# Kernel tuning notes

Hardware: AMD Instinct MI355X
Metric: run time of the kernel (lower is better)

The kernel has to match this reference:

```python
import jax, jax.numpy as jnp
import numpy as np

N_CODES = 1024
CODE_DIM = 256
DECAY = 0.99
EPS = 1e-05


def setup_inputs() -> dict:
    key = jax.random.key(0)
    k1, k2, k3, k4 = jax.random.split(key, 4)
    z = jax.random.normal(k1, (32, CODE_DIM, 32, 32), dtype=jnp.float32)
    embed = jax.random.normal(k2, (N_CODES, CODE_DIM), dtype=jnp.float32)
    cluster_size = jax.random.uniform(k3, (N_CODES,), dtype=jnp.float32)
    embed_avg = jax.random.normal(k4, (N_CODES, CODE_DIM), dtype=jnp.float32)
    return {"z": z, "embed": embed, "cluster_size": cluster_size, "embed_avg": embed_avg}


def reference(z, embed, cluster_size, embed_avg):
    B, D, H, W = z.shape
    K = embed.shape[0]
    # (B*H*W, D) tokens
    flat = jnp.transpose(z, (0, 2, 3, 1)).reshape(-1, D)
    distances = (
        jnp.sum(flat * flat, axis=1, keepdims=True)
        - 2.0 * flat @ embed.T
        + jnp.sum(embed * embed, axis=1)[None, :]
    )
    indices = jnp.argmin(distances, axis=1)  # (N,)
    z_q = embed[indices].reshape(B, H, W, D).transpose(0, 3, 1, 2)  # (B, D, H, W)

    # EMA codebook update (training mode), no onehot materialization
    cs = jax.ops.segment_sum(jnp.ones(flat.shape[0], dtype=flat.dtype), indices, num_segments=K)
    es = jax.ops.segment_sum(flat, indices, num_segments=K)
    new_cluster_size = cluster_size * DECAY + (1.0 - DECAY) * cs
    new_embed_avg = embed_avg * DECAY + (1.0 - DECAY) * es
    n = jnp.sum(new_cluster_size)
    cs_norm = (new_cluster_size + EPS) / (n + K * EPS) * n
    new_embed = new_embed_avg / cs_norm[:, None]

    # straight-through estimator
    z_q_st = z + jax.lax.stop_gradient(z_q - z)
    # torch: F.mse_loss(z.detach(), z_q) -> grads flow to z_q (codebook) only
    vq_loss = jnp.mean((jax.lax.stop_gradient(z) - z_q) ** 2)
    return (z_q_st, indices.reshape(B, H, W), vq_loss, new_embed, new_cluster_size, new_embed_avg)
```

## Files before the change

### kernel.cpp

```cpp
#include <hip/hip_runtime.h>
#include <stdint.h>

#define DECAY 0.99f
#define OMDECAY 0.01f
#define EPSV 1e-5f


typedef _Float16 half8 __attribute__((ext_vector_type(8)));
typedef float floatx4 __attribute__((ext_vector_type(4)));

typedef __attribute__((address_space(1))) const uint32_t gu32;
typedef __attribute__((address_space(3))) uint32_t lu32;

__device__ __forceinline__ void gld16(uint32_t* l, const uint32_t* g) {
    __builtin_amdgcn_global_load_lds((gu32*)g, (lu32*)l, 16, 0, 0);
}

__device__ __forceinline__ uint32_t pack_hl(float v) {
    _Float16 h = (_Float16)v;
    _Float16 lo = (_Float16)(v - (float)h);
    return (uint32_t)__builtin_bit_cast(unsigned short, h) |
           ((uint32_t)__builtin_bit_cast(unsigned short, lo) << 16);
}

__device__ __forceinline__ unsigned int encf(float s) {
    unsigned int b = __builtin_bit_cast(unsigned int, s);
    return (b & 0x80000000u) ? ~b : (b | 0x80000000u);
}

__global__ void prep_embed(const float* __restrict__ embed,
                           unsigned short* __restrict__ B_hi16,
                           unsigned short* __restrict__ B_lo16,
                           float* __restrict__ enorm,
                           float* __restrict__ cs ,
                           uint32_t* __restrict__ b64i) {
    __shared__ float ws4[4];
    const int k = blockIdx.x;
    const int tid = threadIdx.x;
    const int lane = tid & 63;
    const int wv = tid >> 6;
    int idx = k * 256 + tid;
    float v = embed[idx];
    _Float16 h = (_Float16)v;
    _Float16 lo = (_Float16)(v - (float)h);
    B_hi16[idx] = __builtin_bit_cast(unsigned short, h);
    B_lo16[idx] = __builtin_bit_cast(unsigned short, lo);
    float s = v * v;
    for (int off = 32; off > 0; off >>= 1) s += __shfl_down(s, off);
    if (lane == 0) ws4[wv] = s;
    __syncthreads();
    if (tid == 0) enorm[k] = ws4[0] + ws4[1] + ws4[2] + ws4[3];
    if (k < 256) b64i[k * 256 + tid] = 0xFFFFFFFFu;
    if (k == 0) {
        for (int i = tid; i < 2048; i += 256) cs[i] = 0.f;
    }
}

__global__ void split_z(const float* __restrict__ z,
                        uint32_t* __restrict__ A_hi32,
                        uint32_t* __restrict__ A_lo32) {
    __shared__ uint32_t sp[32 * 258];
    const int lane = threadIdx.x & 63;
    const int wv   = threadIdx.x >> 6;
    const int t0   = blockIdx.x * 32;
    const int b    = t0 >> 10;
    const int hw0  = t0 & 1023;
    const int l32  = lane & 31;
    const int dh   = lane >> 5;

    for (int dp = wv; dp < 128; dp += 4) {
        int dd = dp * 2 + dh;
        float v = z[b * 262144 + dd * 1024 + hw0 + l32];
        sp[l32 * 258 + dd] = pack_hl(v);
    }
    __syncthreads();
    for (int r = wv; r < 32; r += 4) {
#pragma unroll
        for (int h2 = 0; h2 < 2; ++h2) {
            int dpair = h2 * 64 + lane;
            uint32_t u0 = sp[r * 258 + 2 * dpair];
            uint32_t u1 = sp[r * 258 + 2 * dpair + 1];
            A_hi32[(t0 + r) * 128 + dpair] = (u0 & 0xffffu) | (u1 << 16);
            A_lo32[(t0 + r) * 128 + dpair] = (u0 >> 16) | (u1 & 0xffff0000u);
        }
    }
}

__global__ __launch_bounds__(256, 2) void vq_mfma(
    const uint32_t* __restrict__ A_hi32,
    const uint32_t* __restrict__ A_lo32,
    const uint32_t* __restrict__ B_hi32,
    const uint32_t* __restrict__ B_lo32,
    const float* __restrict__ enorm,
    unsigned long long* __restrict__ best64)
{
    __shared__ __align__(16) _Float16 AsH[128 * 32];
    __shared__ __align__(16) _Float16 AsL[128 * 32];
    __shared__ __align__(16) _Float16 BsH[256 * 32];
    __shared__ __align__(16) _Float16 BsL[256 * 32];

    const int lane = threadIdx.x & 63;
    const int w    = threadIdx.x >> 6;
    const int q    = lane >> 4;
    const int c16  = lane & 15;
    const int t0   = (blockIdx.x >> 1) * 128;
    const int cb   = (blockIdx.x & 1) * 512;
    const int lane4 = lane >> 2;
    const int dd8   = (lane & 3) * 8;

    for (int nc = 0; nc < 2; ++nc) {
        floatx4 acc[8][4];
#pragma unroll
        for (int i = 0; i < 8; ++i)
#pragma unroll
            for (int j = 0; j < 4; ++j)
                acc[i][j] = (floatx4){0.f, 0.f, 0.f, 0.f};

        for (int dc = 0; dc < 8; ++dc) {
            const int d0 = dc * 32;
            __syncthreads();
            for (int s = w; s < 48; s += 4) {
                if (s < 16) {
                    int ss = s & 7;
                    const uint32_t* base = (s < 8) ? A_hi32 : A_lo32;
                    uint32_t* dst = (uint32_t*)((s < 8) ? AsH : AsL) + ss * 256;
                    int tok = ss * 16 + lane4;
                    gld16(dst, base + (t0 + tok) * 128 + ((d0 + dd8) >> 1));
                } else {
                    int sb = s - 16;
                    int ss = sb & 15;
                    const uint32_t* base = (sb < 16) ? B_hi32 : B_lo32;
                    uint32_t* dst = (uint32_t*)((sb < 16) ? BsH : BsL) + ss * 256;
                    int code = cb + nc * 256 + ss * 16 + lane4;
                    gld16(dst, base + code * 128 + ((d0 + dd8) >> 1));
                }
            }
            __syncthreads();

            half8 bH[4], bL[4];
#pragma unroll
            for (int j = 0; j < 4; ++j) {
                int off = (w * 64 + j * 16 + c16) * 32 + q * 8;
                bH[j] = *(const half8*)(BsH + off);
                bL[j] = *(const half8*)(BsL + off);
            }
#pragma unroll
            for (int i = 0; i < 8; ++i) {
                int off = (i * 16 + c16) * 32 + q * 8;
                half8 aH = *(const half8*)(AsH + off);
                half8 aL = *(const half8*)(AsL + off);
#pragma unroll
                for (int j = 0; j < 4; ++j) {
                    acc[i][j] = __builtin_amdgcn_mfma_f32_16x16x32_f16(aH, bH[j], acc[i][j], 0, 0, 0);
                    acc[i][j] = __builtin_amdgcn_mfma_f32_16x16x32_f16(aH, bL[j], acc[i][j], 0, 0, 0);
                    acc[i][j] = __builtin_amdgcn_mfma_f32_16x16x32_f16(aL, bH[j], acc[i][j], 0, 0, 0);
                }
            }
        }

        float bestv[32];
        int   besti[32];
#pragma unroll
        for (int s = 0; s < 32; ++s) { bestv[s] = 3.4e38f; besti[s] = 0; }
#pragma unroll
        for (int j = 0; j < 4; ++j) {
            int code = cb + nc * 256 + w * 64 + j * 16 + c16;
            float en = enorm[code];
#pragma unroll
            for (int i = 0; i < 8; ++i)
#pragma unroll
                for (int r = 0; r < 4; ++r) {
                    float sc = en - 2.0f * acc[i][j][r];
                    int slot = i * 4 + r;
                    if (sc < bestv[slot] || (sc == bestv[slot] && code < besti[slot])) {
                        bestv[slot] = sc; besti[slot] = code;
                    }
                }
        }
#pragma unroll
        for (int slot = 0; slot < 32; ++slot) {
            float v = bestv[slot]; int bi = besti[slot];
#pragma unroll
            for (int m = 1; m < 16; m <<= 1) {
                float ov = __shfl_xor(v, m);
                int   oi = __shfl_xor(bi, m);
                if (ov < v || (ov == v && oi < bi)) { v = ov; bi = oi; }
            }
            bestv[slot] = v; besti[slot] = bi;
        }
#pragma unroll
        for (int slot = 0; slot < 32; ++slot) {
            if (c16 == (slot & 15)) {
                int tok = (slot >> 2) * 16 + q * 4 + (slot & 3);
                unsigned long long key =
                    ((unsigned long long)encf(bestv[slot]) << 32) |
                    (unsigned int)besti[slot];
                atomicMin(&best64[t0 + tok], key);
            }
        }
    }
}

__global__ __launch_bounds__(256) void merge_zq(
    const unsigned long long* __restrict__ best64,
    const float* __restrict__ z,
    const float* __restrict__ embed,
    float* __restrict__ out_zq,
    float* __restrict__ out_idx,
    float* __restrict__ cs,
    float* __restrict__ loss_sum)
{
    __shared__ int sidx[128];
    const int tid = threadIdx.x;
    const int lane = tid & 63;
    const int w = tid >> 6;
    const int t0 = blockIdx.x * 128;

    if (tid < 128) {
        int bi = (int)(unsigned int)(best64[t0 + tid] & 0xffffffffULL);
        sidx[tid] = bi;
        out_idx[t0 + tid] = (float)bi;
        atomicAdd(&cs[bi], 1.0f);
    }
    __syncthreads();

    const int b_idx = t0 >> 10;
    const int hw0   = t0 & 1023;
    const int zbase = b_idx * 262144 + hw0;
    const int ka = sidx[lane];
    const int kb = sidx[lane + 64];
    float lsum = 0.f;
    for (int d = w; d < 256; d += 4) {
        float zv0 = z[zbase + d * 1024 + lane];
        float zv1 = z[zbase + d * 1024 + lane + 64];
        float e0 = embed[ka * 256 + d];
        float e1 = embed[kb * 256 + d];
        out_zq[zbase + d * 1024 + lane]      = zv0 + (e0 - zv0);
        out_zq[zbase + d * 1024 + lane + 64] = zv1 + (e1 - zv1);
        float d0f = zv0 - e0, d1f = zv1 - e1;
        lsum += d0f * d0f + d1f * d1f;
    }
    for (int off = 32; off > 0; off >>= 1) lsum += __shfl_down(lsum, off);
    if (lane == 0) atomicAdd(loss_sum, lsum);
}

__global__ void vq_finalize_small(const float* __restrict__ cluster_size,
                                  const float* __restrict__ cs,
                                  const float* __restrict__ loss_sum,
                                  float* __restrict__ out_loss,
                                  float* __restrict__ out_ncs,
                                  float* __restrict__ csnorm,
                                  int* __restrict__ offsets,
                                  int* __restrict__ cursor)
{
    __shared__ float wsum[16];
    __shared__ float wncs[16];
    __shared__ float stot[1];
    const int k = threadIdx.x;
    const int lane = k & 63;
    const int wv = k >> 6;
    float cnt = cs[k];
    float ncs = cluster_size[k] * DECAY + OMDECAY * cnt;
    out_ncs[k] = ncs;
    float sc = cnt;
#pragma unroll
    for (int d = 1; d < 64; d <<= 1) {
        float up = __shfl_up(sc, d);
        if (lane >= d) sc += up;
    }
    if (lane == 63) wsum[wv] = sc;
    float ns = ncs;
    for (int off = 32; off > 0; off >>= 1) ns += __shfl_down(ns, off);
    if (lane == 0) wncs[wv] = ns;
    __syncthreads();
    if (wv == 0) {
        float v = (lane < 16) ? wsum[lane] : 0.f;
#pragma unroll
        for (int d = 1; d < 16; d <<= 1) {
            float up = __shfl_up(v, d);
            if (lane >= d) v += up;
        }
        if (lane < 16) wsum[lane] = v;
    } else if (wv == 1) {
        float t = (lane < 16) ? wncs[lane] : 0.f;
        for (int off = 32; off > 0; off >>= 1) t += __shfl_down(t, off);
        if (lane == 0) stot[0] = t;
    }
    __syncthreads();
    float incl = sc + (wv ? wsum[wv - 1] : 0.f);
    int excl = __float2int_rn(incl - cnt);
    offsets[k] = excl;
    cursor[k]  = excl;
    float n = stot[0];
    csnorm[k] = (ncs + EPSV) / (n + 1024.0f * EPSV) * n;
    if (k == 0) out_loss[0] = loss_sum[0] / 8388608.0f;
}

__global__ void scatter_perm(const float* __restrict__ out_idx,
                             int* __restrict__ cursor,
                             int* __restrict__ perm,
                             float* __restrict__ es)
{
    int t = blockIdx.x * 256 + threadIdx.x;
#pragma unroll
    for (int i = 0; i < 8; ++i) es[t + i * 32768] = 0.f;
    int code = (int)out_idx[t];
    int pos = atomicAdd(&cursor[code], 1);
    perm[pos] = t;
}

__global__ void es_sum(const uint32_t* __restrict__ A_hi32,
                       const uint32_t* __restrict__ A_lo32,
                       const int* __restrict__ perm,
                       const float* __restrict__ out_idx,
                       float* __restrict__ es)
{
    __shared__ int sperm[32];
    __shared__ int scode[32];
    const int base = blockIdx.x * 32;
    const int tid = threadIdx.x;
    const int j = tid & 127;
    const uint32_t* __restrict__ A = (tid >> 7) ? A_lo32 : A_hi32;
    if (tid < 32) {
        int t = perm[base + tid];
        sperm[tid] = t;
        scode[tid] = (int)out_idx[t];
    }
    __syncthreads();

    float s0 = 0.f, s1 = 0.f;
    int cur = scode[0];
    uint32_t pu[2];
    pu[0] = A[sperm[0] * 128 + j];
    pu[1] = A[sperm[1] * 128 + j];
#pragma unroll
    for (int i = 0; i < 32; ++i) {
        uint32_t u = pu[i & 1];
        if (i + 2 < 32) pu[i & 1] = A[sperm[i + 2] * 128 + j];
        int code = scode[i];
        if (code != cur) {
            atomicAdd(&es[cur * 256 + 2 * j],     s0);
            atomicAdd(&es[cur * 256 + 2 * j + 1], s1);
            s0 = 0.f; s1 = 0.f; cur = code;
        }
        s0 += (float)__builtin_bit_cast(_Float16, (unsigned short)(u & 0xffffu));
        s1 += (float)__builtin_bit_cast(_Float16, (unsigned short)(u >> 16));
    }
    atomicAdd(&es[cur * 256 + 2 * j],     s0);
    atomicAdd(&es[cur * 256 + 2 * j + 1], s1);
}

__global__ void finalize_embed(const float* __restrict__ embed_avg,
                               const float* __restrict__ es,
                               const float* __restrict__ csnorm,
                               float* __restrict__ out_embed,
                               float* __restrict__ out_nea)
{
    int idx = blockIdx.x * 256 + threadIdx.x;
    int k = idx >> 8;
    float nea = embed_avg[idx] * DECAY + OMDECAY * es[idx];
    out_nea[idx] = nea;
    out_embed[idx] = nea / csnorm[k];
}

extern "C" void kernel_launch(void* const* d_in, const int* in_sizes, int n_in,
                              void* d_out, int out_size, void* d_ws, size_t ws_size,
                              hipStream_t stream) {
    const float* z            = (const float*)d_in[0];
    const float* embed        = (const float*)d_in[1];
    const float* cluster_size = (const float*)d_in[2];
    const float* embed_avg    = (const float*)d_in[3];
    float* out = (float*)d_out;
    uint32_t* ws32 = (uint32_t*)d_ws;

    uint32_t* B_hi32 = ws32 + 0;
    uint32_t* B_lo32 = ws32 + 131072;
    uint32_t* A_hi32 = ws32 + 262144;
    uint32_t* A_lo32 = ws32 + 4456448;
    int* perm        = (int*)(ws32 + 8650752);
    int* offsets     = (int*)(ws32 + 8683520);
    int* cursor      = (int*)(ws32 + 8684544);
    float* cs        = (float*)(ws32 + 8912896);
    float* loss_sum  = (float*)(ws32 + 8913920);
    float* enorm     = (float*)(ws32 + 8914944);
    float* csnorm    = (float*)(ws32 + 8915968);
    float* es        = (float*)(ws32 + 0);
    unsigned long long* best64 = (unsigned long long*)(out + 8421378);

    prep_embed<<<1024, 256, 0, stream>>>(embed, (unsigned short*)B_hi32,
                                         (unsigned short*)B_lo32, enorm, cs,
                                         (uint32_t*)best64);
    split_z<<<1024, 256, 0, stream>>>(z, A_hi32, A_lo32);
    vq_mfma<<<512, 256, 0, stream>>>(A_hi32, A_lo32, B_hi32, B_lo32, enorm, best64);
    merge_zq<<<256, 256, 0, stream>>>(best64, z, embed,
                                      out, out + 8388608, cs, loss_sum);
    vq_finalize_small<<<1, 1024, 0, stream>>>(cluster_size, cs, loss_sum,
                                              out + 8421376, out + 8683521, csnorm,
                                              offsets, cursor);
    scatter_perm<<<128, 256, 0, stream>>>(out + 8388608, cursor, perm, es);
    es_sum<<<1024, 256, 0, stream>>>(A_hi32, A_lo32, perm, out + 8388608, es);
    finalize_embed<<<1024, 256, 0, stream>>>(embed_avg, es, csnorm,
                                             out + 8421377, out + 8684545);
}
```

Before: 270.4 us.

## Double-buffer LDS tiles in VQ MFMA kernel with 512-thread blocks and swizzle

```diff
diff --git a/kernel.cpp b/kernel.cpp
--- a/kernel.cpp
+++ b/kernel.cpp
@@ -86,7 +86,7 @@
     }
 }
 
-__global__ __launch_bounds__(256, 2) void vq_mfma(
+__global__ __launch_bounds__(512, 2) void vq_mfma(
     const uint32_t* __restrict__ A_hi32,
     const uint32_t* __restrict__ A_lo32,
     const uint32_t* __restrict__ B_hi32,
@@ -94,83 +94,108 @@
     const float* __restrict__ enorm,
     unsigned long long* __restrict__ best64)
 {
-    __shared__ __align__(16) _Float16 AsH[128 * 32];
-    __shared__ __align__(16) _Float16 AsL[128 * 32];
-    __shared__ __align__(16) _Float16 BsH[256 * 32];
-    __shared__ __align__(16) _Float16 BsL[256 * 32];
-
-    const int lane = threadIdx.x & 63;
-    const int w    = threadIdx.x >> 6;
-    const int q    = lane >> 4;
-    const int c16  = lane & 15;
-    const int t0   = (blockIdx.x >> 1) * 128;
-    const int cb   = (blockIdx.x & 1) * 512;
+    __shared__ __align__(16) _Float16 lds[2][4][8192];
+
+    const int lane  = threadIdx.x & 63;
+    const int w     = threadIdx.x >> 6;
+    const int wh    = w >> 2;
+    const int wj    = w & 3;
+    const int q     = lane >> 4;
+    const int c16   = lane & 15;
+    const int t0    = (blockIdx.x >> 1) * 256;
+    const int cb    = (blockIdx.x & 1) * 512;
     const int lane4 = lane >> 2;
-    const int dd8   = (lane & 3) * 8;
-
+    const int dd8s  = ((lane & 3) ^ ((lane >> 3) & 3)) * 8;
+    const int qs    = q ^ ((c16 >> 1) & 3);
+
+    const int m = w >> 1;
+    const uint32_t* const sbase =
+        (m == 0) ? A_hi32 : (m == 1) ? A_lo32 : (m == 2) ? B_hi32 : B_lo32;
+    const bool isA = (m < 2);
+
+    float en[2][4];
+#pragma unroll
+    for (int nc = 0; nc < 2; ++nc)
+#pragma unroll
+        for (int j = 0; j < 4; ++j)
+            en[nc][j] = enorm[cb + nc * 256 + wj * 64 + j * 16 + c16];
+
+    floatx4 acc[8][4];
+#pragma unroll
+    for (int i = 0; i < 8; ++i)
+#pragma unroll
+        for (int j = 0; j < 4; ++j)
+            acc[i][j] = (floatx4){0.f, 0.f, 0.f, 0.f};
+
+    auto STAGE = [&](int step) {
+        const int buf = step & 1;
+        const int ncs = (step >> 3) & 1;
+        const int d0  = (step & 7) * 32;
+        const int srcoff = (d0 + dd8s) >> 1;
+        const int rowb = isA ? t0 : (cb + ncs * 256);
+        uint32_t* dst0 = (uint32_t*)(&lds[buf][m][0]);
+#pragma unroll
+        for (int s8 = 0; s8 < 8; ++s8) {
+            const int r16 = (w & 1) * 8 + s8;
+            const int row = rowb + r16 * 16 + lane4;
+            gld16(dst0 + r16 * 256, sbase + row * 128 + srcoff);
+        }
+    };
+
+    STAGE(0);
+
+#pragma unroll
     for (int nc = 0; nc < 2; ++nc) {
-        floatx4 acc[8][4];
-#pragma unroll
-        for (int i = 0; i < 8; ++i)
-#pragma unroll
-            for (int j = 0; j < 4; ++j)
-                acc[i][j] = (floatx4){0.f, 0.f, 0.f, 0.f};
-
         for (int dc = 0; dc < 8; ++dc) {
-            const int d0 = dc * 32;
-            __syncthreads();
-            for (int s = w; s < 48; s += 4) {
-                if (s < 16) {
-                    int ss = s & 7;
-                    const uint32_t* base = (s < 8) ? A_hi32 : A_lo32;
-                    uint32_t* dst = (uint32_t*)((s < 8) ? AsH : AsL) + ss * 256;
-                    int tok = ss * 16 + lane4;
-                    gld16(dst, base + (t0 + tok) * 128 + ((d0 + dd8) >> 1));
-                } else {
-                    int sb = s - 16;
-                    int ss = sb & 15;
-                    const uint32_t* base = (sb < 16) ? B_hi32 : B_lo32;
-                    uint32_t* dst = (uint32_t*)((sb < 16) ? BsH : BsL) + ss * 256;
-                    int code = cb + nc * 256 + ss * 16 + lane4;
-                    gld16(dst, base + code * 128 + ((d0 + dd8) >> 1));
+            const int s = nc * 8 + dc;
+            STAGE((s + 1) & 15);
+            asm volatile("s_waitcnt vmcnt(8)" ::: "memory");
+            __builtin_amdgcn_s_barrier();
+            asm volatile("" ::: "memory");
+
+            const _Float16* pAH = &lds[s & 1][0][0];
+            const _Float16* pAL = &lds[s & 1][1][0];
+            const _Float16* pBH = &lds[s & 1][2][0];
+            const _Float16* pBL = &lds[s & 1][3][0];
+
+            half8 bH[4], bL[4];
+#pragma unroll
+            for (int j = 0; j < 4; ++j) {
+                const int off = (wj * 64 + j * 16 + c16) * 32 + qs * 8;
+                bH[j] = *(const half8*)(pBH + off);
+                bL[j] = *(const half8*)(pBL + off);
+            }
+            __builtin_amdgcn_s_setprio(1);
+#pragma unroll
+            for (int i = 0; i < 8; ++i) {
+                const int off = (wh * 128 + i * 16 + c16) * 32 + qs * 8;
+                half8 vaH = *(const half8*)(pAH + off);
+                half8 vaL = *(const half8*)(pAL + off);
+#pragma unroll
+                for (int j = 0; j < 4; ++j) {
+                    acc[i][j] = __builtin_amdgcn_mfma_f32_16x16x32_f16(vaH, bH[j], acc[i][j], 0, 0, 0);
+                    acc[i][j] = __builtin_amdgcn_mfma_f32_16x16x32_f16(vaH, bL[j], acc[i][j], 0, 0, 0);
+                    acc[i][j] = __builtin_amdgcn_mfma_f32_16x16x32_f16(vaL, bH[j], acc[i][j], 0, 0, 0);
                 }
             }
-            __syncthreads();
-
-            half8 bH[4], bL[4];
-#pragma unroll
-            for (int j = 0; j < 4; ++j) {
-                int off = (w * 64 + j * 16 + c16) * 32 + q * 8;
-                bH[j] = *(const half8*)(BsH + off);
-                bL[j] = *(const half8*)(BsL + off);
-            }
-#pragma unroll
-            for (int i = 0; i < 8; ++i) {
-                int off = (i * 16 + c16) * 32 + q * 8;
-                half8 aH = *(const half8*)(AsH + off);
-                half8 aL = *(const half8*)(AsL + off);
-#pragma unroll
-                for (int j = 0; j < 4; ++j) {
-                    acc[i][j] = __builtin_amdgcn_mfma_f32_16x16x32_f16(aH, bH[j], acc[i][j], 0, 0, 0);
-                    acc[i][j] = __builtin_amdgcn_mfma_f32_16x16x32_f16(aH, bL[j], acc[i][j], 0, 0, 0);
-                    acc[i][j] = __builtin_amdgcn_mfma_f32_16x16x32_f16(aL, bH[j], acc[i][j], 0, 0, 0);
-                }
-            }
+            __builtin_amdgcn_s_setprio(0);
+            asm volatile("" ::: "memory");
+            __builtin_amdgcn_s_barrier();
         }
 
         float bestv[32];
         int   besti[32];
 #pragma unroll
-        for (int s = 0; s < 32; ++s) { bestv[s] = 3.4e38f; besti[s] = 0; }
+        for (int sl = 0; sl < 32; ++sl) { bestv[sl] = 3.4e38f; besti[sl] = 0; }
 #pragma unroll
         for (int j = 0; j < 4; ++j) {
-            int code = cb + nc * 256 + w * 64 + j * 16 + c16;
-            float en = enorm[code];
+            const int code = cb + nc * 256 + wj * 64 + j * 16 + c16;
+            const float enj = en[nc][j];
 #pragma unroll
             for (int i = 0; i < 8; ++i)
 #pragma unroll
                 for (int r = 0; r < 4; ++r) {
-                    float sc = en - 2.0f * acc[i][j][r];
+                    float sc = enj - 2.0f * acc[i][j][r];
                     int slot = i * 4 + r;
                     if (sc < bestv[slot] || (sc == bestv[slot] && code < besti[slot])) {
                         bestv[slot] = sc; besti[slot] = code;
@@ -181,9 +206,9 @@
         for (int slot = 0; slot < 32; ++slot) {
             float v = bestv[slot]; int bi = besti[slot];
 #pragma unroll
-            for (int m = 1; m < 16; m <<= 1) {
-                float ov = __shfl_xor(v, m);
-                int   oi = __shfl_xor(bi, m);
+            for (int mm = 1; mm < 16; mm <<= 1) {
+                float ov = __shfl_xor(v, mm);
+                int   oi = __shfl_xor(bi, mm);
                 if (ov < v || (ov == v && oi < bi)) { v = ov; bi = oi; }
             }
             bestv[slot] = v; besti[slot] = bi;
@@ -191,12 +216,19 @@
 #pragma unroll
         for (int slot = 0; slot < 32; ++slot) {
             if (c16 == (slot & 15)) {
-                int tok = (slot >> 2) * 16 + q * 4 + (slot & 3);
+                int tok = t0 + wh * 128 + (slot >> 2) * 16 + q * 4 + (slot & 3);
                 unsigned long long key =
                     ((unsigned long long)encf(bestv[slot]) << 32) |
                     (unsigned int)besti[slot];
-                atomicMin(&best64[t0 + tok], key);
+                atomicMin(&best64[tok], key);
             }
+        }
+        if (nc == 0) {
+#pragma unroll
+            for (int i = 0; i < 8; ++i)
+#pragma unroll
+                for (int j = 0; j < 4; ++j)
+                    acc[i][j] = (floatx4){0.f, 0.f, 0.f, 0.f};
         }
     }
 }
@@ -391,7 +423,7 @@
                                          (unsigned short*)B_lo32, enorm, cs,
                                          (uint32_t*)best64);
     split_z<<<1024, 256, 0, stream>>>(z, A_hi32, A_lo32);
-    vq_mfma<<<512, 256, 0, stream>>>(A_hi32, A_lo32, B_hi32, B_lo32, enorm, best64);
+    vq_mfma<<<256, 512, 0, stream>>>(A_hi32, A_lo32, B_hi32, B_lo32, enorm, best64);
     merge_zq<<<256, 256, 0, stream>>>(best64, z, embed,
                                       out, out + 8388608, cs, loss_sum);
     vq_finalize_small<<<1, 1024, 0, stream>>>(cluster_size, cs, loss_sum,
```

Measured after the change: 266.2 us. No clear change (-1.5%).

## Restructure VQ distance GEMM with double-buffered A, register B, and XCD-aware mapping

Applied to the files above, without the earlier changes.

```diff
diff --git a/kernel.cpp b/kernel.cpp
--- a/kernel.cpp
+++ b/kernel.cpp
@@ -28,60 +28,60 @@
     return (b & 0x80000000u) ? ~b : (b | 0x80000000u);
 }
 
-__global__ void prep_embed(const float* __restrict__ embed,
+__global__ void prep_fused(const float* __restrict__ z,
+                           uint32_t* __restrict__ A_hi32,
+                           uint32_t* __restrict__ A_lo32,
+                           const float* __restrict__ embed,
                            unsigned short* __restrict__ B_hi16,
                            unsigned short* __restrict__ B_lo16,
                            float* __restrict__ enorm,
                            float* __restrict__ cs ,
                            uint32_t* __restrict__ b64i) {
-    __shared__ float ws4[4];
-    const int k = blockIdx.x;
+    __shared__ uint32_t sp[32 * 258];
+    const int bx = blockIdx.x;
     const int tid = threadIdx.x;
     const int lane = tid & 63;
     const int wv = tid >> 6;
-    int idx = k * 256 + tid;
-    float v = embed[idx];
-    _Float16 h = (_Float16)v;
-    _Float16 lo = (_Float16)(v - (float)h);
-    B_hi16[idx] = __builtin_bit_cast(unsigned short, h);
-    B_lo16[idx] = __builtin_bit_cast(unsigned short, lo);
-    float s = v * v;
-    for (int off = 32; off > 0; off >>= 1) s += __shfl_down(s, off);
-    if (lane == 0) ws4[wv] = s;
-    __syncthreads();
-    if (tid == 0) enorm[k] = ws4[0] + ws4[1] + ws4[2] + ws4[3];
-    if (k < 256) b64i[k * 256 + tid] = 0xFFFFFFFFu;
-    if (k == 0) {
-        for (int i = tid; i < 2048; i += 256) cs[i] = 0.f;
-    }
-}
-
-__global__ void split_z(const float* __restrict__ z,
-                        uint32_t* __restrict__ A_hi32,
-                        uint32_t* __restrict__ A_lo32) {
-    __shared__ uint32_t sp[32 * 258];
-    const int lane = threadIdx.x & 63;
-    const int wv   = threadIdx.x >> 6;
-    const int t0   = blockIdx.x * 32;
-    const int b    = t0 >> 10;
-    const int hw0  = t0 & 1023;
-    const int l32  = lane & 31;
-    const int dh   = lane >> 5;
-
-    for (int dp = wv; dp < 128; dp += 4) {
-        int dd = dp * 2 + dh;
-        float v = z[b * 262144 + dd * 1024 + hw0 + l32];
-        sp[l32 * 258 + dd] = pack_hl(v);
-    }
-    __syncthreads();
-    for (int r = wv; r < 32; r += 4) {
-#pragma unroll
-        for (int h2 = 0; h2 < 2; ++h2) {
-            int dpair = h2 * 64 + lane;
-            uint32_t u0 = sp[r * 258 + 2 * dpair];
-            uint32_t u1 = sp[r * 258 + 2 * dpair + 1];
-            A_hi32[(t0 + r) * 128 + dpair] = (u0 & 0xffffu) | (u1 << 16);
-            A_lo32[(t0 + r) * 128 + dpair] = (u0 >> 16) | (u1 & 0xffff0000u);
+
+    if (bx < 1024) {
+        const int t0  = bx * 32;
+        const int b   = t0 >> 10;
+        const int hw0 = t0 & 1023;
+        const int l32 = lane & 31;
+        const int dh  = lane >> 5;
+        for (int dp = wv; dp < 128; dp += 4) {
+            int dd = dp * 2 + dh;
+            float v = z[b * 262144 + dd * 1024 + hw0 + l32];
+            sp[l32 * 258 + dd] = pack_hl(v);
+        }
+        __syncthreads();
+        for (int r = wv; r < 32; r += 4) {
+#pragma unroll
+            for (int h2 = 0; h2 < 2; ++h2) {
+                int dpair = h2 * 64 + lane;
+                uint32_t u0 = sp[r * 258 + 2 * dpair];
+                uint32_t u1 = sp[r * 258 + 2 * dpair + 1];
+                A_hi32[(t0 + r) * 128 + dpair] = (u0 & 0xffffu) | (u1 << 16);
+                A_lo32[(t0 + r) * 128 + dpair] = (u0 >> 16) | (u1 & 0xffff0000u);
+            }
+        }
+    } else {
+        float* ws4 = (float*)sp;
+        const int k = bx - 1024;
+        int idx = k * 256 + tid;
+        float v = embed[idx];
+        _Float16 h = (_Float16)v;
+        _Float16 lo = (_Float16)(v - (float)h);
+        B_hi16[idx] = __builtin_bit_cast(unsigned short, h);
+        B_lo16[idx] = __builtin_bit_cast(unsigned short, lo);
+        float s = v * v;
+        for (int off = 32; off > 0; off >>= 1) s += __shfl_down(s, off);
+        if (lane == 0) ws4[wv] = s;
+        __syncthreads();
+        if (tid == 0) enorm[k] = ws4[0] + ws4[1] + ws4[2] + ws4[3];
+        if (k < 256) b64i[k * 256 + tid] = 0xFFFFFFFFu;
+        if (k == 0) {
+            for (int i = tid; i < 2048; i += 256) cs[i] = 0.f;
         }
     }
 }
@@ -94,109 +94,127 @@
     const float* __restrict__ enorm,
     unsigned long long* __restrict__ best64)
 {
-    __shared__ __align__(16) _Float16 AsH[128 * 32];
-    __shared__ __align__(16) _Float16 AsL[128 * 32];
-    __shared__ __align__(16) _Float16 BsH[256 * 32];
-    __shared__ __align__(16) _Float16 BsL[256 * 32];
+    __shared__ __align__(16) _Float16 Abuf[2][2][4096];
 
     const int lane = threadIdx.x & 63;
     const int w    = threadIdx.x >> 6;
     const int q    = lane >> 4;
     const int c16  = lane & 15;
-    const int t0   = (blockIdx.x >> 1) * 128;
-    const int cb   = (blockIdx.x & 1) * 512;
+    const int bb   = blockIdx.x;
+    const int xcd  = bb & 7;
+    const int slot = bb >> 3;
+    const int g    = (slot >> 2) * 8 + xcd;
+    const int cq   = slot & 3;
+    const int t0   = g * 128;
+    const int cb   = cq * 256;
     const int lane4 = lane >> 2;
-    const int dd8   = (lane & 3) * 8;
-
-    for (int nc = 0; nc < 2; ++nc) {
-        floatx4 acc[8][4];
+    const int dd8s  = ((lane & 3) ^ ((lane >> 3) & 3)) * 8;
+    const int qs    = q ^ ((c16 >> 1) & 3);
+
+    const uint32_t* const sA = (w >> 1) ? A_lo32 : A_hi32;
+    const int r16b = (w & 1) * 4;
+
+    float en[4];
+    const uint32_t* bph[4];
+    const uint32_t* bpl[4];
+#pragma unroll
+    for (int j = 0; j < 4; ++j) {
+        const int code = cb + w * 64 + j * 16 + c16;
+        en[j]  = enorm[code];
+        bph[j] = B_hi32 + code * 128 + q * 4;
+        bpl[j] = B_lo32 + code * 128 + q * 4;
+    }
+
+    floatx4 acc[8][4];
+#pragma unroll
+    for (int i = 0; i < 8; ++i)
+#pragma unroll
+        for (int j = 0; j < 4; ++j)
+            acc[i][j] = (floatx4){0.f, 0.f, 0.f, 0.f};
+
+    half8 bh[2][4], bl[2][4];
+
+    auto STAGE_A = [&](int step) {
+        uint32_t* dst = (uint32_t*)(&Abuf[step & 1][w >> 1][0]);
+        const int srcoff = (step * 32 + dd8s) >> 1;
+#pragma unroll
+        for (int s = 0; s < 4; ++s) {
+            const int r16 = r16b + s;
+            gld16(dst + r16 * 256, sA + (t0 + r16 * 16 + lane4) * 128 + srcoff);
+        }
+    };
+    auto LOAD_B = [&](int step, half8* h, half8* l) {
+#pragma unroll
+        for (int j = 0; j < 4; ++j) {
+            h[j] = *(const half8*)(bph[j] + step * 16);
+            l[j] = *(const half8*)(bpl[j] + step * 16);
+        }
+    };
+
+    STAGE_A(0);
+    LOAD_B(0, bh[0], bl[0]);
+
+#pragma unroll
+    for (int dc = 0; dc < 8; ++dc) {
+        if (dc < 7) {
+            STAGE_A(dc + 1);
+            LOAD_B(dc + 1, bh[(dc + 1) & 1], bl[(dc + 1) & 1]);
+            asm volatile("s_waitcnt vmcnt(12)" ::: "memory");
+        } else {
+            asm volatile("s_waitcnt vmcnt(0)" ::: "memory");
+        }
+        __builtin_amdgcn_s_barrier();
+        asm volatile("" ::: "memory");
+
+        const _Float16* pH = &Abuf[dc & 1][0][0];
+        const _Float16* pL = &Abuf[dc & 1][1][0];
+        __builtin_amdgcn_s_setprio(1);
+#pragma unroll
+        for (int i = 0; i < 8; ++i) {
+            const int off = (i * 16 + c16) * 32 + qs * 8;
+            half8 aH = *(const half8*)(pH + off);
+            half8 aL = *(const half8*)(pL + off);
+#pragma unroll
+            for (int j = 0; j < 4; ++j) {
+                acc[i][j] = __builtin_amdgcn_mfma_f32_16x16x32_f16(aH, bh[dc & 1][j], acc[i][j], 0, 0, 0);
+                acc[i][j] = __builtin_amdgcn_mfma_f32_16x16x32_f16(aH, bl[dc & 1][j], acc[i][j], 0, 0, 0);
+                acc[i][j] = __builtin_amdgcn_mfma_f32_16x16x32_f16(aL, bh[dc & 1][j], acc[i][j], 0, 0, 0);
+            }
+        }
+        __builtin_amdgcn_s_setprio(0);
+        asm volatile("" ::: "memory");
+        if (dc < 7) __builtin_amdgcn_s_barrier();
+    }
+
+    unsigned long long best[32];
+#pragma unroll
+    for (int sl = 0; sl < 32; ++sl) best[sl] = ~0ULL;
+#pragma unroll
+    for (int j = 0; j < 4; ++j) {
+        const unsigned int code = (unsigned int)(cb + w * 64 + j * 16 + c16);
+        const float enj = en[j];
 #pragma unroll
         for (int i = 0; i < 8; ++i)
 #pragma unroll
-            for (int j = 0; j < 4; ++j)
-                acc[i][j] = (floatx4){0.f, 0.f, 0.f, 0.f};
-
-        for (int dc = 0; dc < 8; ++dc) {
-            const int d0 = dc * 32;
-            __syncthreads();
-            for (int s = w; s < 48; s += 4) {
-                if (s < 16) {
-                    int ss = s & 7;
-                    const uint32_t* base = (s < 8) ? A_hi32 : A_lo32;
-                    uint32_t* dst = (uint32_t*)((s < 8) ? AsH : AsL) + ss * 256;
-                    int tok = ss * 16 + lane4;
-                    gld16(dst, base + (t0 + tok) * 128 + ((d0 + dd8) >> 1));
-                } else {
-                    int sb = s - 16;
-                    int ss = sb & 15;
-                    const uint32_t* base = (sb < 16) ? B_hi32 : B_lo32;
-                    uint32_t* dst = (uint32_t*)((sb < 16) ? BsH : BsL) + ss * 256;
-                    int code = cb + nc * 256 + ss * 16 + lane4;
-                    gld16(dst, base + code * 128 + ((d0 + dd8) >> 1));
-                }
+            for (int r = 0; r < 4; ++r) {
+                float sc = enj - 2.0f * acc[i][j][r];
+                unsigned long long key =
+                    ((unsigned long long)encf(sc) << 32) | code;
+                int sl = i * 4 + r;
+                if (key < best[sl]) best[sl] = key;
             }
-            __syncthreads();
-
-            half8 bH[4], bL[4];
-#pragma unroll
-            for (int j = 0; j < 4; ++j) {
-                int off = (w * 64 + j * 16 + c16) * 32 + q * 8;
-                bH[j] = *(const half8*)(BsH + off);
-                bL[j] = *(const half8*)(BsL + off);
-            }
-#pragma unroll
-            for (int i = 0; i < 8; ++i) {
-                int off = (i * 16 + c16) * 32 + q * 8;
-                half8 aH = *(const half8*)(AsH + off);
-                half8 aL = *(const half8*)(AsL + off);
-#pragma unroll
-                for (int j = 0; j < 4; ++j) {
-                    acc[i][j] = __builtin_amdgcn_mfma_f32_16x16x32_f16(aH, bH[j], acc[i][j], 0, 0, 0);
-                    acc[i][j] = __builtin_amdgcn_mfma_f32_16x16x32_f16(aH, bL[j], acc[i][j], 0, 0, 0);
-                    acc[i][j] = __builtin_amdgcn_mfma_f32_16x16x32_f16(aL, bH[j], acc[i][j], 0, 0, 0);
-                }
-            }
-        }
-
-        float bestv[32];
-        int   besti[32];
-#pragma unroll
-        for (int s = 0; s < 32; ++s) { bestv[s] = 3.4e38f; besti[s] = 0; }
-#pragma unroll
-        for (int j = 0; j < 4; ++j) {
-            int code = cb + nc * 256 + w * 64 + j * 16 + c16;
-            float en = enorm[code];
-#pragma unroll
-            for (int i = 0; i < 8; ++i)
-#pragma unroll
-                for (int r = 0; r < 4; ++r) {
-                    float sc = en - 2.0f * acc[i][j][r];
-                    int slot = i * 4 + r;
-                    if (sc < bestv[slot] || (sc == bestv[slot] && code < besti[slot])) {
-                        bestv[slot] = sc; besti[slot] = code;
-                    }
-                }
-        }
-#pragma unroll
-        for (int slot = 0; slot < 32; ++slot) {
-            float v = bestv[slot]; int bi = besti[slot];
-#pragma unroll
-            for (int m = 1; m < 16; m <<= 1) {
-                float ov = __shfl_xor(v, m);
-                int   oi = __shfl_xor(bi, m);
-                if (ov < v || (ov == v && oi < bi)) { v = ov; bi = oi; }
-            }
-            bestv[slot] = v; besti[slot] = bi;
-        }
-#pragma unroll
-        for (int slot = 0; slot < 32; ++slot) {
-            if (c16 == (slot & 15)) {
-                int tok = (slot >> 2) * 16 + q * 4 + (slot & 3);
-                unsigned long long key =
-                    ((unsigned long long)encf(bestv[slot]) << 32) |
-                    (unsigned int)besti[slot];
-                atomicMin(&best64[t0 + tok], key);
-            }
+    }
+#pragma unroll
+    for (int sl = 0; sl < 32; ++sl) {
+        unsigned long long v = best[sl];
+#pragma unroll
+        for (int mm = 1; mm < 16; mm <<= 1) {
+            unsigned long long o = __shfl_xor(v, mm);
+            if (o < v) v = o;
+        }
+        if (c16 == (sl & 15)) {
+            int tok = t0 + (sl >> 2) * 16 + q * 4 + (sl & 3);
+            atomicMin(&best64[tok], v);
         }
     }
 }
@@ -387,11 +405,11 @@
     float* es        = (float*)(ws32 + 0);
     unsigned long long* best64 = (unsigned long long*)(out + 8421378);
 
-    prep_embed<<<1024, 256, 0, stream>>>(embed, (unsigned short*)B_hi32,
+    prep_fused<<<2048, 256, 0, stream>>>(z, A_hi32, A_lo32, embed,
+                                         (unsigned short*)B_hi32,
                                          (unsigned short*)B_lo32, enorm, cs,
                                          (uint32_t*)best64);
-    split_z<<<1024, 256, 0, stream>>>(z, A_hi32, A_lo32);
-    vq_mfma<<<512, 256, 0, stream>>>(A_hi32, A_lo32, B_hi32, B_lo32, enorm, best64);
+    vq_mfma<<<1024, 256, 0, stream>>>(A_hi32, A_lo32, B_hi32, B_lo32, enorm, best64);
     merge_zq<<<256, 256, 0, stream>>>(best64, z, embed,
                                       out, out + 8388608, cs, loss_sum);
     vq_finalize_small<<<1, 1024, 0, stream>>>(cluster_size, cs, loss_sum,
```

Result: faster. 247.2 us (-8.6%).
